# Optimization experiments

Measured on AMD Instinct MI355X. Metric: run time of the kernel, lower is better.

Reference implementation:

```python
import jax, jax.numpy as jnp
import numpy as np

PATCH = 32          # feature map is PATCH x PATCH, N = PATCH**2 tokens
HEADS = 8
HD = 24             # head_dim (hardcoded in Block -> Cluster3D)
P = 4               # proposal_w = proposal_h = 4 -> 16 cluster centers
EPS_NORM = 1e-12    # F.normalize eps
LN_EPS = 1e-5


def _layernorm(x, g, b):
    m = x.mean(-1, keepdims=True)
    v = ((x - m) ** 2).mean(-1, keepdims=True)
    return (x - m) / jnp.sqrt(v + LN_EPS) * g + b


def _cluster3d(xn, f_w, f_b, v_w, v_b, alpha, beta, proj_w, proj_b):
    # xn: [B, N, D] with tokens laid out row-major over a PATCH x PATCH grid
    B, N, D = xn.shape
    M = P * P
    feat = xn @ f_w.T + f_b   # [B, N, HEADS*HD]  (1x1 conv f)
    val = xn @ v_w.T + v_b    # [B, N, HEADS*HD]  (1x1 conv v)

    def to_heads(t):  # channel layout is (e c): head-major
        return t.reshape(B, N, HEADS, HD).transpose(0, 2, 1, 3).reshape(B * HEADS, N, HD)

    fh = to_heads(feat)       # [Bh, N, HD]
    vh = to_heads(val)

    def pool(t):  # AdaptiveAvgPool to (P, P) over the PATCH x PATCH grid
        g = t.reshape(-1, P, PATCH // P, P, PATCH // P, HD).mean(axis=(2, 4))
        return g.reshape(-1, M, HD)

    centers = pool(fh)        # [Bh, M, HD]
    vcenters = pool(vh)       # [Bh, M, HD]

    cn = centers / jnp.clip(jnp.linalg.norm(centers, axis=-1, keepdims=True), EPS_NORM)
    fn = fh / jnp.clip(jnp.linalg.norm(fh, axis=-1, keepdims=True), EPS_NORM)
    sim = beta + alpha * jnp.einsum('bmc,bnc->bmn', cn, fn)   # [Bh, M, N]
    sim = jnp.where(sim >= 0, sim, 0.2 * sim)                 # LeakyReLU(0.2); dropout eval=identity

    # hard top-1 assignment of each token to its best center
    idx = jnp.argmax(sim, axis=1)                              # [Bh, N]
    mask = jax.nn.one_hot(idx, M, dtype=sim.dtype).transpose(0, 2, 1)  # [Bh, M, N]
    mask = jax.lax.stop_gradient(mask)
    sim = sim * mask

    # aggregate tokens into centers, then dispatch back
    agg = (jnp.einsum('bmn,bnc->bmc', sim, vh) + vcenters) / (mask.sum(-1, keepdims=True) + 1.0)
    out = jnp.einsum('bmn,bmc->bnc', sim, agg)                 # [Bh, N, HD]

    out = out.reshape(B, HEADS, N, HD).transpose(0, 2, 1, 3).reshape(B, N, HEADS * HD)
    return out @ proj_w.T + proj_b                             # [B, N, D]


def setup_inputs() -> dict:
    key = jax.random.key(0)
    ks = jax.random.split(key, 8)
    B, N, D, HID, HH = 64, PATCH * PATCH, 512, 2048, HEADS * HD
    s = 0.02
    return {
        'x': jax.random.normal(ks[0], (B, N, D), jnp.float32),
        'ln1_g': jnp.ones((D,), jnp.float32),
        'ln1_b': jnp.zeros((D,), jnp.float32),
        'f_w': jax.random.normal(ks[1], (HH, D), jnp.float32) * s,
        'f_b': jnp.zeros((HH,), jnp.float32),
        'v_w': jax.random.normal(ks[2], (HH, D), jnp.float32) * s,
        'v_b': jnp.zeros((HH,), jnp.float32),
        'sim_alpha': jnp.ones((1,), jnp.float32),
        'sim_beta': jnp.zeros((1,), jnp.float32),
        'proj_w': jax.random.normal(ks[3], (D, HH), jnp.float32) * s,
        'proj_b': jnp.zeros((D,), jnp.float32),
        'ln2_g': jnp.ones((D,), jnp.float32),
        'ln2_b': jnp.zeros((D,), jnp.float32),
        'fc1_w': jax.random.normal(ks[4], (HID, D), jnp.float32) * s,
        'fc1_b': jnp.zeros((HID,), jnp.float32),
        'fc2_w': jax.random.normal(ks[5], (D, HID), jnp.float32) * s,
        'fc2_b': jnp.zeros((D,), jnp.float32),
    }


def reference(x, ln1_g, ln1_b, f_w, f_b, v_w, v_b, sim_alpha, sim_beta,
              proj_w, proj_b, ln2_g, ln2_b, fc1_w, fc1_b, fc2_w, fc2_b):
    x = x + _cluster3d(_layernorm(x, ln1_g, ln1_b), f_w, f_b, v_w, v_b,
                       sim_alpha, sim_beta, proj_w, proj_b)
    h = _layernorm(x, ln2_g, ln2_b)
    h = jax.nn.gelu(h @ fc1_w.T + fc1_b, approximate=False)
    x = x + (h @ fc2_w.T + fc2_b)
    return x
```

## Files before the change

### kernel.cpp

```cpp
#include <hip/hip_runtime.h>


typedef __attribute__((ext_vector_type(8))) short short8;
typedef __attribute__((ext_vector_type(4))) short short4v;
typedef __attribute__((ext_vector_type(4))) float floatx4;

static __device__ __forceinline__ short f2bf(float f) {
  union { float f; unsigned u; } a; a.f = f;
  unsigned r = a.u + 0x7fffu + ((a.u >> 16) & 1u);
  return (short)(r >> 16);
}

static __device__ __forceinline__ void gload_lds16(const short* g, short* l) {
  __builtin_amdgcn_global_load_lds(
      (const __attribute__((address_space(1))) void*)g,
      (__attribute__((address_space(3))) void*)l, 16, 0, 0);
}

__global__ __launch_bounds__(256) void cvt_f32_bf16(
    const float* __restrict__ in, short* __restrict__ out, int n4)
{
  int i = blockIdx.x * 256 + threadIdx.x;
  if (i >= n4) return;
  float4 v = reinterpret_cast<const float4*>(in)[i];
  short4v o;
  o[0] = f2bf(v.x); o[1] = f2bf(v.y); o[2] = f2bf(v.z); o[3] = f2bf(v.w);
  reinterpret_cast<short4v*>(out)[i] = o;
}

__global__ __launch_bounds__(256) void ln_kernel(
    const float* __restrict__ x, const float* __restrict__ g,
    const float* __restrict__ b, short* __restrict__ out)
{
  const int wave = threadIdx.x >> 6, lane = threadIdx.x & 63;
  const size_t row = (size_t)blockIdx.x * 4 + wave;
  const float* xr = x + row * 512;
  const int c = lane * 8;
  float4 v0 = *reinterpret_cast<const float4*>(xr + c);
  float4 v1 = *reinterpret_cast<const float4*>(xr + c + 4);
  float xs[8] = {v0.x, v0.y, v0.z, v0.w, v1.x, v1.y, v1.z, v1.w};
  float s = 0.f, q = 0.f;
#pragma unroll
  for (int k = 0; k < 8; ++k) { s += xs[k]; q += xs[k] * xs[k]; }
#pragma unroll
  for (int off = 32; off; off >>= 1) {
    s += __shfl_xor(s, off);
    q += __shfl_xor(q, off);
  }
  const float mean = s * (1.0f / 512.0f);
  const float var  = q * (1.0f / 512.0f) - mean * mean;
  const float rstd = rsqrtf(var + 1e-5f);
  short8 o;
#pragma unroll
  for (int k = 0; k < 8; ++k)
    o[k] = f2bf((xs[k] - mean) * rstd * g[c + k] + b[c + k]);
  *reinterpret_cast<short8*>(out + row * 512 + c) = o;
}

template<int BM, int BN, int WM, int WN, int EPI>
__global__ __launch_bounds__(256, 2) void gemm_bt(
    const short* __restrict__ A, const short* __restrict__ W,
    const float* __restrict__ bias, const float* __restrict__ resid,
    float* __restrict__ Cf, short* __restrict__ Cb,
    const int N, const int K)
{
  constexpr int BK = 32;
  __shared__ short Al[BM * BK];
  __shared__ short Wl[BN * BK];
  const int tid  = threadIdx.x;
  const int wave = tid >> 6;
  const int lane = tid & 63;
  constexpr int WCOLS = BN / WN;
  const int wm = (wave / WCOLS) * WM;
  const int wn = (wave % WCOLS) * WN;
  constexpr int MI = WM / 16, NJ = WN / 16;
  const int row0 = blockIdx.x * BM;
  const int col0 = blockIdx.y * BN;
  const int r  = lane & 15;
  const int kc = lane >> 4;

  floatx4 acc[MI][NJ];
#pragma unroll
  for (int i = 0; i < MI; ++i)
#pragma unroll
    for (int j = 0; j < NJ; ++j)
      acc[i][j] = (floatx4){0.f, 0.f, 0.f, 0.f};

  const short* Ab = A + (size_t)row0 * K;
  const short* Wb = W + (size_t)col0 * K;

  for (int k0 = 0; k0 < K; k0 += BK) {
#pragma unroll
    for (int u = 0; u < BM / 64; ++u) {
      const int cc = u * 256 + tid;
      const int rr = cc >> 2, sl = cc & 3;
      const int co = sl ^ ((rr >> 1) & 3);
      gload_lds16(Ab + (size_t)rr * K + k0 + co * 8, &Al[cc * 8]);
    }
#pragma unroll
    for (int u = 0; u < BN / 64; ++u) {
      const int cc = u * 256 + tid;
      const int rr = cc >> 2, sl = cc & 3;
      const int co = sl ^ ((rr >> 1) & 3);
      gload_lds16(Wb + (size_t)rr * K + k0 + co * 8, &Wl[cc * 8]);
    }
    __syncthreads();
    short8 af[MI], wfr[NJ];
#pragma unroll
    for (int i = 0; i < MI; ++i) {
      const int rt = wm + 16 * i + r;
      af[i] = *reinterpret_cast<const short8*>(
          &Al[rt * BK + ((kc ^ ((rt >> 1) & 3)) << 3)]);
    }
#pragma unroll
    for (int j = 0; j < NJ; ++j) {
      const int rt = wn + 16 * j + r;
      wfr[j] = *reinterpret_cast<const short8*>(
          &Wl[rt * BK + ((kc ^ ((rt >> 1) & 3)) << 3)]);
    }
#pragma unroll
    for (int i = 0; i < MI; ++i)
#pragma unroll
      for (int j = 0; j < NJ; ++j)
        acc[i][j] = __builtin_amdgcn_mfma_f32_16x16x32_bf16(
            af[i], wfr[j], acc[i][j], 0, 0, 0);
    __syncthreads();
  }

#pragma unroll
  for (int i = 0; i < MI; ++i) {
#pragma unroll
    for (int j = 0; j < NJ; ++j) {
      const int col = col0 + wn + 16 * j + r;
      const float bv = bias[col];
#pragma unroll
      for (int t = 0; t < 4; ++t) {
        const int rowi = row0 + wm + 16 * i + (lane >> 4) * 4 + t;
        const size_t offo = (size_t)rowi * N + col;
        float v = acc[i][j][t] + bv;
        if (EPI == 0) {
          Cf[offo] = v;
        } else if (EPI == 1) {
          Cf[offo] = v + resid[offo];
        } else {
          v = 0.5f * v * (1.0f + erff(v * 0.70710678118654752f));
          Cb[offo] = f2bf(v);
        }
      }
    }
  }
}

__global__ __launch_bounds__(384) void pool_kernel(
    const float* __restrict__ feat, const float* __restrict__ val,
    float* __restrict__ cn, float* __restrict__ vcent)
{
  const int bh = blockIdx.x;
  const int b = bh >> 3, h = bh & 7;
  const int t = threadIdx.x;
  const int m = t / 24, c = t % 24;
  const int cy = m >> 2, cx = m & 3;
  const size_t base = (size_t)b * 1024 * 192 + h * 24 + c;
  float sf = 0.f, sv = 0.f;
  for (int dy = 0; dy < 8; ++dy) {
    const int ny = (cy * 8 + dy) * 32 + cx * 8;
    for (int dx = 0; dx < 8; ++dx) {
      const size_t off = base + (size_t)(ny + dx) * 192;
      sf += feat[off];
      sv += val[off];
    }
  }
  sf *= (1.0f / 64.0f); sv *= (1.0f / 64.0f);
  __shared__ float cent[16][24];
  cent[m][c] = sf;
  vcent[(size_t)bh * 384 + t] = sv;
  __syncthreads();
  float nrm = 0.f;
#pragma unroll
  for (int k = 0; k < 24; ++k) nrm += cent[m][k] * cent[m][k];
  nrm = fmaxf(sqrtf(nrm), 1e-12f);
  cn[(size_t)bh * 384 + t] = sf / nrm;
}

__global__ __launch_bounds__(256) void sim_kernel(
    const float* __restrict__ feat, const float* __restrict__ cn,
    const float* __restrict__ alpha_p, const float* __restrict__ beta_p,
    float* __restrict__ sval, int* __restrict__ sidx)
{
  const int bh = blockIdx.y;
  const int b = bh >> 3, h = bh & 7;
  __shared__ float cs[384];
  for (int i = threadIdx.x; i < 384; i += 256) cs[i] = cn[(size_t)bh * 384 + i];
  __syncthreads();
  const int n = blockIdx.x * 256 + threadIdx.x;
  const float* f = feat + (size_t)(b * 1024 + n) * 192 + h * 24;
  float v[24];
#pragma unroll
  for (int k = 0; k < 24; k += 4) {
    float4 t4 = *reinterpret_cast<const float4*>(f + k);
    v[k] = t4.x; v[k + 1] = t4.y; v[k + 2] = t4.z; v[k + 3] = t4.w;
  }
  float q = 0.f;
#pragma unroll
  for (int k = 0; k < 24; ++k) q += v[k] * v[k];
  const float inv = 1.0f / fmaxf(sqrtf(q), 1e-12f);
  const float alpha = alpha_p[0], beta = beta_p[0];
  float best = -3.4e38f; int bi = 0;
#pragma unroll
  for (int m = 0; m < 16; ++m) {
    float d = 0.f;
#pragma unroll
    for (int k = 0; k < 24; ++k) d += cs[m * 24 + k] * v[k];
    float s = beta + alpha * (d * inv);
    s = (s < 0.f) ? 0.2f * s : s;
    if (s > best) { best = s; bi = m; }
  }
  sval[(size_t)bh * 1024 + n] = best;
  sidx[(size_t)bh * 1024 + n] = bi;
}

__global__ __launch_bounds__(256) void agg_kernel(
    const float* __restrict__ val, const float* __restrict__ vcent,
    const float* __restrict__ sval, const int* __restrict__ sidx,
    float* __restrict__ agg)
{
  const int bh = blockIdx.x;
  const int b = bh >> 3, h = bh & 7;
  __shared__ float acc[384];
  __shared__ float cnt[16];
  for (int i = threadIdx.x; i < 384; i += 256) acc[i] = 0.f;
  if (threadIdx.x < 16) cnt[threadIdx.x] = 0.f;
  __syncthreads();
  for (int n = threadIdx.x; n < 1024; n += 256) {
    const float s = sval[(size_t)bh * 1024 + n];
    const int m = sidx[(size_t)bh * 1024 + n];
    atomicAdd(&cnt[m], 1.0f);
    const float* vv = val + (size_t)(b * 1024 + n) * 192 + h * 24;
#pragma unroll
    for (int k = 0; k < 24; ++k) atomicAdd(&acc[m * 24 + k], s * vv[k]);
  }
  __syncthreads();
  for (int i = threadIdx.x; i < 384; i += 256) {
    const int m = i / 24;
    agg[(size_t)bh * 384 + i] = (acc[i] + vcent[(size_t)bh * 384 + i]) / (cnt[m] + 1.0f);
  }
}

__global__ __launch_bounds__(256) void dispatch_kernel(
    const float* __restrict__ sval, const int* __restrict__ sidx,
    const float* __restrict__ agg, short* __restrict__ o)
{
  const int g = blockIdx.x * 256 + threadIdx.x;
  const int h = g & 7, n = (g >> 3) & 1023, b = g >> 13;
  const int bh = b * 8 + h;
  const float s = sval[(size_t)bh * 1024 + n];
  const int m = sidx[(size_t)bh * 1024 + n];
  const float* a = agg + (size_t)bh * 384 + m * 24;
  short* op = o + ((size_t)(b * 1024 + n)) * 192 + h * 24;
  short8 pack[3];
#pragma unroll
  for (int k = 0; k < 24; ++k) pack[k >> 3][k & 7] = f2bf(s * a[k]);
  short8* dst = reinterpret_cast<short8*>(op);
  dst[0] = pack[0]; dst[1] = pack[1]; dst[2] = pack[2];
}

extern "C" void kernel_launch(void* const* d_in, const int* in_sizes, int n_in,
                              void* d_out, int out_size, void* d_ws, size_t ws_size,
                              hipStream_t stream)
{
  const float* x      = (const float*)d_in[0];
  const float* ln1_g  = (const float*)d_in[1];
  const float* ln1_b  = (const float*)d_in[2];
  const float* f_w    = (const float*)d_in[3];
  const float* f_b    = (const float*)d_in[4];
  const float* v_w    = (const float*)d_in[5];
  const float* v_b    = (const float*)d_in[6];
  const float* alpha  = (const float*)d_in[7];
  const float* beta   = (const float*)d_in[8];
  const float* proj_w = (const float*)d_in[9];
  const float* proj_b = (const float*)d_in[10];
  const float* ln2_g  = (const float*)d_in[11];
  const float* ln2_b  = (const float*)d_in[12];
  const float* fc1_w  = (const float*)d_in[13];
  const float* fc1_b  = (const float*)d_in[14];
  const float* fc2_w  = (const float*)d_in[15];
  const float* fc2_b  = (const float*)d_in[16];
  float* out = (float*)d_out;

  char* ws = (char*)d_ws;
  size_t off = 0;
  auto alloc = [&](size_t bytes) -> char* {
    char* p = ws + off;
    off = (off + bytes + 255) & ~(size_t)255;
    return p;
  };
  short* xn   = (short*)alloc(67108864);
  float* feat = (float*)alloc(50331648);
  float* val  = (float*)alloc(50331648);
  short* o    = (short*)alloc(25165824);
  float* x1   = (float*)alloc(134217728);
  short* wf   = (short*)alloc(196608);
  short* wv   = (short*)alloc(196608);
  short* wp   = (short*)alloc(196608);
  short* w1   = (short*)alloc(2097152);
  short* w2   = (short*)alloc(2097152);
  float* cnb  = (float*)alloc(786432);
  float* vcb  = (float*)alloc(786432);
  float* agb  = (float*)alloc(786432);
  float* svb  = (float*)alloc(2097152);
  int*   sib  = (int*)  alloc(2097152);
  short* h  = (short*)feat;
  short* h1 = xn;

  cvt_f32_bf16<<<96,   256, 0, stream>>>(f_w,    wf, 24576);
  cvt_f32_bf16<<<96,   256, 0, stream>>>(v_w,    wv, 24576);
  cvt_f32_bf16<<<96,   256, 0, stream>>>(proj_w, wp, 24576);
  cvt_f32_bf16<<<1024, 256, 0, stream>>>(fc1_w,  w1, 262144);
  cvt_f32_bf16<<<1024, 256, 0, stream>>>(fc2_w,  w2, 262144);

  ln_kernel<<<16384, 256, 0, stream>>>(x, ln1_g, ln1_b, xn);

  gemm_bt<128, 64, 64, 32, 0><<<dim3(512, 3), 256, 0, stream>>>(
      xn, wf, f_b, nullptr, feat, nullptr, 192, 512);
  gemm_bt<128, 64, 64, 32, 0><<<dim3(512, 3), 256, 0, stream>>>(
      xn, wv, v_b, nullptr, val, nullptr, 192, 512);

  pool_kernel<<<512, 384, 0, stream>>>(feat, val, cnb, vcb);
  sim_kernel<<<dim3(4, 512), 256, 0, stream>>>(feat, cnb, alpha, beta, svb, sib);
  agg_kernel<<<512, 256, 0, stream>>>(val, vcb, svb, sib, agb);
  dispatch_kernel<<<2048, 256, 0, stream>>>(svb, sib, agb, o);

  gemm_bt<128, 128, 64, 64, 1><<<dim3(512, 4), 256, 0, stream>>>(
      o, wp, proj_b, x, x1, nullptr, 512, 192);

  ln_kernel<<<16384, 256, 0, stream>>>(x1, ln2_g, ln2_b, h);

  for (int c = 0; c < 4; ++c) {
    const short* hA = h + (size_t)c * 16384 * 512;
    gemm_bt<128, 128, 64, 64, 2><<<dim3(128, 16), 256, 0, stream>>>(
        hA, w1, fc1_b, nullptr, nullptr, h1, 2048, 512);
    gemm_bt<128, 64, 64, 32, 1><<<dim3(128, 8), 256, 0, stream>>>(
        h1, w2, fc2_b, x1 + (size_t)c * 16384 * 512,
        out + (size_t)c * 16384 * 512, nullptr, 512, 2048);
  }
  (void)in_sizes; (void)n_in; (void)out_size; (void)ws_size;
}
```

Measured before the change: 1.024 ms.

## Double-buffer GEMM LDS tiles and enlarge f/v projection tiles

Adds a two-stage LDS ping-pong to the bf16 GEMM so the global-to-LDS load of the next K tile is issued before the MFMA work on the current tile, with one barrier per iteration instead of two. Load source/destination addresses and LDS fragment offsets are precomputed outside the K loop. The f and v projection GEMMs switch to 256x64 tiles with 64x64 wave tiles. This doubles LDS use per block, which may lower occupancy, and the per-wave accumulators grow for the projection kernels.

```diff
diff --git a/kernel.cpp b/kernel.cpp
--- a/kernel.cpp
+++ b/kernel.cpp
@@ -65,8 +65,11 @@
     const int N, const int K)
 {
   constexpr int BK = 32;
-  __shared__ short Al[BM * BK];
-  __shared__ short Wl[BN * BK];
+  constexpr int T  = 256;
+  constexpr int AC = (BM * BK / 8) / T;
+  constexpr int WC = (BN * BK / 8) / T;
+  __shared__ short Al[2][BM * BK];
+  __shared__ short Wl[2][BN * BK];
   const int tid  = threadIdx.x;
   const int wave = tid >> 6;
   const int lane = tid & 63;
@@ -89,35 +92,55 @@
   const short* Ab = A + (size_t)row0 * K;
   const short* Wb = W + (size_t)col0 * K;
 
-  for (int k0 = 0; k0 < K; k0 += BK) {
-#pragma unroll
-    for (int u = 0; u < BM / 64; ++u) {
-      const int cc = u * 256 + tid;
-      const int rr = cc >> 2, sl = cc & 3;
-      const int co = sl ^ ((rr >> 1) & 3);
-      gload_lds16(Ab + (size_t)rr * K + k0 + co * 8, &Al[cc * 8]);
-    }
-#pragma unroll
-    for (int u = 0; u < BN / 64; ++u) {
-      const int cc = u * 256 + tid;
-      const int rr = cc >> 2, sl = cc & 3;
-      const int co = sl ^ ((rr >> 1) & 3);
-      gload_lds16(Wb + (size_t)rr * K + k0 + co * 8, &Wl[cc * 8]);
-    }
-    __syncthreads();
+  const short* aSrc[AC]; int aDst[AC];
+#pragma unroll
+  for (int u = 0; u < AC; ++u) {
+    const int cc = u * T + tid;
+    const int rr = cc >> 2, sl = cc & 3;
+    const int co = sl ^ ((rr >> 1) & 3);
+    aSrc[u] = Ab + (size_t)rr * K + co * 8;
+    aDst[u] = cc * 8;
+  }
+  const short* wSrc[WC]; int wDst[WC];
+#pragma unroll
+  for (int u = 0; u < WC; ++u) {
+    const int cc = u * T + tid;
+    const int rr = cc >> 2, sl = cc & 3;
+    const int co = sl ^ ((rr >> 1) & 3);
+    wSrc[u] = Wb + (size_t)rr * K + co * 8;
+    wDst[u] = cc * 8;
+  }
+  int aOff[MI], wOff[NJ];
+#pragma unroll
+  for (int i = 0; i < MI; ++i) {
+    const int rt = wm + 16 * i + r;
+    aOff[i] = rt * BK + ((kc ^ ((rt >> 1) & 3)) << 3);
+  }
+#pragma unroll
+  for (int j = 0; j < NJ; ++j) {
+    const int rt = wn + 16 * j + r;
+    wOff[j] = rt * BK + ((kc ^ ((rt >> 1) & 3)) << 3);
+  }
+
+  auto stage = [&](int buf, int k0) {
+#pragma unroll
+    for (int u = 0; u < AC; ++u) gload_lds16(aSrc[u] + k0, &Al[buf][aDst[u]]);
+#pragma unroll
+    for (int u = 0; u < WC; ++u) gload_lds16(wSrc[u] + k0, &Wl[buf][wDst[u]]);
+  };
+
+  stage(0, 0);
+  __syncthreads();
+  int cur = 0;
+  for (int k0 = BK; k0 <= K; k0 += BK) {
+    if (k0 < K) stage(cur ^ 1, k0);
     short8 af[MI], wfr[NJ];
 #pragma unroll
-    for (int i = 0; i < MI; ++i) {
-      const int rt = wm + 16 * i + r;
-      af[i] = *reinterpret_cast<const short8*>(
-          &Al[rt * BK + ((kc ^ ((rt >> 1) & 3)) << 3)]);
-    }
-#pragma unroll
-    for (int j = 0; j < NJ; ++j) {
-      const int rt = wn + 16 * j + r;
-      wfr[j] = *reinterpret_cast<const short8*>(
-          &Wl[rt * BK + ((kc ^ ((rt >> 1) & 3)) << 3)]);
-    }
+    for (int i = 0; i < MI; ++i)
+      af[i] = *reinterpret_cast<const short8*>(&Al[cur][aOff[i]]);
+#pragma unroll
+    for (int j = 0; j < NJ; ++j)
+      wfr[j] = *reinterpret_cast<const short8*>(&Wl[cur][wOff[j]]);
 #pragma unroll
     for (int i = 0; i < MI; ++i)
 #pragma unroll
@@ -125,6 +148,7 @@
         acc[i][j] = __builtin_amdgcn_mfma_f32_16x16x32_bf16(
             af[i], wfr[j], acc[i][j], 0, 0, 0);
     __syncthreads();
+    cur ^= 1;
   }
 
 #pragma unroll
@@ -320,9 +344,9 @@
 
   ln_kernel<<<16384, 256, 0, stream>>>(x, ln1_g, ln1_b, xn);
 
-  gemm_bt<128, 64, 64, 32, 0><<<dim3(512, 3), 256, 0, stream>>>(
+  gemm_bt<256, 64, 64, 64, 0><<<dim3(256, 3), 256, 0, stream>>>(
       xn, wf, f_b, nullptr, feat, nullptr, 192, 512);
-  gemm_bt<128, 64, 64, 32, 0><<<dim3(512, 3), 256, 0, stream>>>(
+  gemm_bt<256, 64, 64, 64, 0><<<dim3(256, 3), 256, 0, stream>>>(
       xn, wv, v_b, nullptr, val, nullptr, 192, 512);
 
   pool_kernel<<<512, 384, 0, stream>>>(feat, val, cnb, vcb);
```

Result: faster. 1.002 ms (-2.1%).
